# Performance work log

Measured on AMD Instinct MI355X. Metric: run time of the kernel, lower is better.

Reference implementation:

```python
import jax, jax.numpy as jnp
import numpy as np

N = 50000
E = 800000
L = 0.7
EPS = 1e-12  # torch F.normalize eps


def setup_inputs() -> dict:
    key = jax.random.key(0)
    k1, k2, k3, k4, k5 = jax.random.split(key, 5)
    x = jax.random.normal(k1, (N, 256), dtype=jnp.float32)
    W = jax.random.normal(k2, (256, 128), dtype=jnp.float32) * 0.05
    b = jax.random.normal(k3, (128,), dtype=jnp.float32) * 0.05
    src = jax.random.randint(k4, (E,), 0, N, dtype=jnp.int32)
    dst = jax.random.randint(k5, (E,), 0, N, dtype=jnp.int32)
    return {"x": x, "W": W, "b": b, "src": src, "dst": dst}


def _mean_agg(h, src, dst, denom):
    # DGL copy_u + mean over in-edges: mean_{e:(u->v)} h[u]; zero for isolated nodes
    s = jax.ops.segment_sum(h[src], dst, num_segments=N)  # [N, D]
    return s / denom


def reference(x, W, b, src, dst):
    # MLP: Linear -> relu -> row-wise L2 normalize
    h = jax.nn.relu(x @ W + b)
    h = h / jnp.maximum(jnp.linalg.norm(h, axis=1, keepdims=True), EPS)
    # in-degree for mean (clamped to 1 so isolated nodes give 0, matching DGL)
    deg = jax.ops.segment_sum(jnp.ones((E,), jnp.float32), dst, num_segments=N)
    denom = jnp.maximum(deg, 1.0)[:, None]  # [N,1]
    neigh1 = _mean_agg(h, src, dst, denom)
    neigh2 = _mean_agg(neigh1, src, dst, denom)
    mean_h = L * neigh1 + (1.0 - L) * neigh2
    return (h, mean_h)
```

## Files before the change

### kernel.cpp

```cpp
#include <hip/hip_runtime.h>

#define D_IN 256
#define D_OUT 128
#define NBINS 256
#define NB 256

typedef short bf16x8 __attribute__((ext_vector_type(8)));
typedef float f32x4 __attribute__((ext_vector_type(4)));

__device__ __forceinline__ unsigned short f2bf(float f) {
    unsigned int u = __float_as_uint(f);
    unsigned int r = (u + 0x7FFFu + ((u >> 16) & 1u)) >> 16;
    return (unsigned short)r;
}
__device__ __forceinline__ unsigned int pack2(float a, float b) {
    return (unsigned int)f2bf(a) | ((unsigned int)f2bf(b) << 16);
}
__device__ __forceinline__ void gload_lds16(const void* g, void* l) {
    __builtin_amdgcn_global_load_lds(
        (const __attribute__((address_space(1))) void*)g,
        (__attribute__((address_space(3))) void*)l, 16, 0, 0);
}

__global__ __launch_bounds__(256) void k_wt_b1(const float* __restrict__ W,
                                               unsigned short* __restrict__ wt,
                                               const int* __restrict__ dst, int E, int epb,
                                               int* __restrict__ blockbase) {
    __shared__ int hist[NBINS];
    int t = threadIdx.x;
    if (t < 128) {
        int idx = blockIdx.x * 128 + t;
        wt[idx] = f2bf(W[(idx & 255) * D_OUT + (idx >> 8)]);
    }
    hist[t] = 0;
    __syncthreads();
    int s = blockIdx.x * epb;
    int e = min(s + epb, E);
    for (int i = s + t; i < e; i += 256)
        atomicAdd(&hist[dst[i] >> 8], 1);
    __syncthreads();
    blockbase[blockIdx.x * NBINS + t] = hist[t];
}

__global__ __launch_bounds__(256) void k_csrmlp(
    const int* __restrict__ src, const int* __restrict__ dst, int E, int epb,
    const int* __restrict__ blockbase, int* __restrict__ coarse_cnt,
    int* __restrict__ coarse_base, int* __restrict__ ebuf,
    const float* __restrict__ x, const unsigned short* __restrict__ wt,
    const float* __restrict__ bias, float* __restrict__ h,
    unsigned char* __restrict__ hq, int n, int nmblk) {
    __shared__ char smem[32768];
    const int tid = threadIdx.x;
    const int bid = blockIdx.x;

    if (bid < NB) {
        int* cur  = (int*)smem;
        int* base = (int*)(smem + 1024);
        int* sd   = (int*)(smem + 2048);
        int run = 0, myprefix = 0;
        #pragma unroll 8
        for (int b = 0; b < NB; ++b) {
            int v = blockbase[b * NBINS + tid];
            if (b == bid) myprefix = run;
            run += v;
        }
        sd[tid] = run;
        cur[tid] = 0;
        __syncthreads();
        for (int off = 1; off < 256; off <<= 1) {
            int v = (tid >= off) ? sd[tid - off] : 0;
            __syncthreads();
            sd[tid] += v;
            __syncthreads();
        }
        int cb_excl = sd[tid] - run;
        base[tid] = cb_excl + myprefix;
        if (bid == 0) { coarse_cnt[tid] = run; coarse_base[tid] = cb_excl; }
        __syncthreads();
        const int s = bid * epb, e = min(s + epb, E);
        for (int i = s + tid; i < e; i += 256) {
            int d = dst[i];
            int bin = d >> 8;
            int p = atomicAdd(&cur[bin], 1);
            ebuf[base[bin] + p] = (src[i] & 0xffff) | ((d & 255) << 16);
        }
        return;
    }

    const int tile = bid - NB;
    if (tile >= nmblk) return;
    float* sx = (float*)smem;
    unsigned short* swc = (unsigned short*)(smem + 16384);
    const int wid  = tid >> 6;
    const int lane = tid & 63;
    const int row0 = tile * 64;

    f32x4 acc[8];
    #pragma unroll
    for (int fn = 0; fn < 8; ++fn) acc[fn] = (f32x4){0.f, 0.f, 0.f, 0.f};

    for (int k0 = 0; k0 < D_IN; k0 += 64) {
        __syncthreads();
        #pragma unroll
        for (int i = 0; i < 4; ++i) {
            int bi = i * 4 + wid;
            int chunk = bi * 64 + lane;
            int r  = chunk >> 4;
            int cs = chunk & 15;
            int grow = row0 + r;
            const float* g = x + (size_t)grow * D_IN + k0 + ((cs ^ (r & 7)) << 2);
            if (grow < n) gload_lds16(g, (char*)sx + bi * 1024);
        }
        #pragma unroll
        for (int i = 0; i < 4; ++i) {
            int bi = i * 4 + wid;
            int chunk = bi * 64 + lane;
            int nr = chunk >> 3;
            int cs = chunk & 7;
            const unsigned short* g = wt + nr * D_IN + k0 + ((cs ^ (nr & 7)) << 3);
            gload_lds16(g, (char*)swc + bi * 1024);
        }
        __syncthreads();

        #pragma unroll
        for (int kk = 0; kk < 2; ++kk) {
            int r  = wid * 16 + (lane & 15);
            int cs = kk * 8 + (lane >> 4) * 2;
            float4 a0 = *reinterpret_cast<const float4*>(sx + r * 64 + ((cs ^ (r & 7)) << 2));
            float4 a1 = *reinterpret_cast<const float4*>(sx + r * 64 + (((cs + 1) ^ (r & 7)) << 2));
            union { unsigned int u[4]; bf16x8 v; } af;
            af.u[0] = pack2(a0.x, a0.y);
            af.u[1] = pack2(a0.z, a0.w);
            af.u[2] = pack2(a1.x, a1.y);
            af.u[3] = pack2(a1.z, a1.w);
            #pragma unroll
            for (int fn = 0; fn < 8; ++fn) {
                int nr = fn * 16 + (lane & 15);
                int cb = kk * 4 + (lane >> 4);
                bf16x8 bfrag = *reinterpret_cast<const bf16x8*>(
                    swc + nr * 64 + ((cb ^ (nr & 7)) << 3));
                acc[fn] = __builtin_amdgcn_mfma_f32_16x16x32_bf16(af.v, bfrag, acc[fn], 0, 0, 0);
            }
        }
    }

    float bias_r[8];
    #pragma unroll
    for (int fn = 0; fn < 8; ++fn) bias_r[fn] = bias[fn * 16 + (lane & 15)];
    const int colbase = lane & 15;
    const int rgrp = lane >> 4;
    #pragma unroll
    for (int reg = 0; reg < 4; ++reg) {
        int grow = row0 + wid * 16 + rgrp * 4 + reg;
        float v[8];
        float ss = 0.f;
        #pragma unroll
        for (int fn = 0; fn < 8; ++fn) {
            float t = fmaxf(acc[fn][reg] + bias_r[fn], 0.f);
            v[fn] = t;
            ss += t * t;
        }
        ss += __shfl_xor(ss, 1);
        ss += __shfl_xor(ss, 2);
        ss += __shfl_xor(ss, 4);
        ss += __shfl_xor(ss, 8);
        float sc = 1.f / fmaxf(sqrtf(ss), 1e-12f);
        if (grow < n) {
            #pragma unroll
            for (int fn = 0; fn < 8; ++fn) {
                float o = v[fn] * sc;
                h[(size_t)grow * D_OUT + fn * 16 + colbase] = o;
                hq[(size_t)grow * D_OUT + fn * 16 + colbase] =
                    (unsigned char)(int)rintf(o * 255.f);
            }
        }
    }
}

__global__ __launch_bounds__(256) void k_b4(const int* __restrict__ ebuf,
                                            const int* __restrict__ coarse_cnt,
                                            const int* __restrict__ coarse_base,
                                            int* __restrict__ deg, int* __restrict__ offs,
                                            int* __restrict__ csr, int n) {
    __shared__ int hist[NBINS];
    __shared__ int loffs[NBINS];
    int t = threadIdx.x;
    int bin = blockIdx.x;
    int base = coarse_base[bin];
    int size = coarse_cnt[bin];
    hist[t] = 0;
    __syncthreads();
    for (int i = t; i < size; i += 256)
        atomicAdd(&hist[(ebuf[base + i] >> 16) & 255], 1);
    __syncthreads();
    int h = hist[t];
    loffs[t] = h;
    __syncthreads();
    for (int off = 1; off < 256; off <<= 1) {
        int v = (t >= off) ? loffs[t - off] : 0;
        __syncthreads();
        loffs[t] += v;
        __syncthreads();
    }
    int excl = loffs[t] - h;
    int gdst = bin * 256 + t;
    if (gdst < n) {
        deg[gdst]  = h;
        offs[gdst] = base + excl;
    }
    __syncthreads();
    hist[t] = excl;
    __syncthreads();
    for (int i = t; i < size; i += 256) {
        int pr = ebuf[base + i];
        int p = atomicAdd(&hist[(pr >> 16) & 255], 1);
        csr[base + p] = pr & 0xffff;
    }
}

__global__ __launch_bounds__(256) void k_agg1(const unsigned char* __restrict__ hq,
                                              const int* __restrict__ offs,
                                              const int* __restrict__ deg,
                                              const int* __restrict__ csr,
                                              unsigned char* __restrict__ n1q, int n) {
    int node = (blockIdx.x * blockDim.x + threadIdx.x) >> 5;
    int sub  = threadIdx.x & 31;
    if (node >= n) return;
    int d = deg[node];
    int s = offs[node], e = s + d;
    unsigned int a0 = 0u, a1 = 0u;
    int i = s;
    for (; i + 7 < e; i += 8) {
        #pragma unroll
        for (int j = 0; j < 8; ++j) {
            int u = csr[i + j];
            unsigned int q = *reinterpret_cast<const unsigned int*>(
                hq + (size_t)u * D_OUT + sub * 4);
            a0 += q & 0x00FF00FFu;
            a1 += (q >> 8) & 0x00FF00FFu;
        }
    }
    for (; i < e; ++i) {
        int u = csr[i];
        unsigned int q = *reinterpret_cast<const unsigned int*>(
            hq + (size_t)u * D_OUT + sub * 4);
        a0 += q & 0x00FF00FFu;
        a1 += (q >> 8) & 0x00FF00FFu;
    }
    float inv = 1.f / (float)max(d, 1);
    unsigned int b0 = (unsigned int)(int)rintf((float)(a0 & 0xffffu) * inv);
    unsigned int b1 = (unsigned int)(int)rintf((float)(a1 & 0xffffu) * inv);
    unsigned int b2 = (unsigned int)(int)rintf((float)(a0 >> 16) * inv);
    unsigned int b3 = (unsigned int)(int)rintf((float)(a1 >> 16) * inv);
    *reinterpret_cast<unsigned int*>(n1q + (size_t)node * D_OUT + sub * 4) =
        b0 | (b1 << 8) | (b2 << 16) | (b3 << 24);
}

__global__ __launch_bounds__(256) void k_agg2(const unsigned char* __restrict__ n1q,
                                              const int* __restrict__ offs,
                                              const int* __restrict__ deg,
                                              const int* __restrict__ csr,
                                              float* __restrict__ out_m, int n) {
    int node = (blockIdx.x * blockDim.x + threadIdx.x) >> 5;
    int sub  = threadIdx.x & 31;
    if (node >= n) return;
    int d = deg[node];
    int s = offs[node], e = s + d;
    unsigned int a0 = 0u, a1 = 0u;
    int i = s;
    for (; i + 7 < e; i += 8) {
        #pragma unroll
        for (int j = 0; j < 8; ++j) {
            int u = csr[i + j];
            unsigned int q = *reinterpret_cast<const unsigned int*>(
                n1q + (size_t)u * D_OUT + sub * 4);
            a0 += q & 0x00FF00FFu;
            a1 += (q >> 8) & 0x00FF00FFu;
        }
    }
    for (; i < e; ++i) {
        int u = csr[i];
        unsigned int q = *reinterpret_cast<const unsigned int*>(
            n1q + (size_t)u * D_OUT + sub * 4);
        a0 += q & 0x00FF00FFu;
        a1 += (q >> 8) & 0x00FF00FFu;
    }
    float inv = 1.f / (float)max(d, 1);
    unsigned int own = *reinterpret_cast<const unsigned int*>(
        n1q + (size_t)node * D_OUT + sub * 4);
    const float s255 = 1.f / 255.f;
    float4 o;
    o.x = (0.7f * (float)(own & 0xffu)         + 0.3f * (float)(a0 & 0xffffu) * inv) * s255;
    o.y = (0.7f * (float)((own >> 8) & 0xffu)  + 0.3f * (float)(a1 & 0xffffu) * inv) * s255;
    o.z = (0.7f * (float)((own >> 16) & 0xffu) + 0.3f * (float)(a0 >> 16) * inv) * s255;
    o.w = (0.7f * (float)(own >> 24)           + 0.3f * (float)(a1 >> 16) * inv) * s255;
    *reinterpret_cast<float4*>(out_m + (size_t)node * D_OUT + sub * 4) = o;
}

static inline size_t align_up(size_t v, size_t a) { return (v + a - 1) & ~(a - 1); }

extern "C" void kernel_launch(void* const* d_in, const int* in_sizes, int n_in,
                              void* d_out, int out_size, void* d_ws, size_t ws_size,
                              hipStream_t stream) {
    const float* x  = (const float*)d_in[0];
    const float* W  = (const float*)d_in[1];
    const float* b  = (const float*)d_in[2];
    const int* src  = (const int*)d_in[3];
    const int* dst  = (const int*)d_in[4];

    const int n = in_sizes[0] / D_IN;
    const int E = in_sizes[3];

    float* out_h = (float*)d_out;
    float* out_m = out_h + (size_t)n * D_OUT;

    char* ws = (char*)d_ws;
    size_t off = 0;
    int* coarse_cnt  = (int*)(ws + off); off = align_up(off + NBINS * 4, 256);
    int* coarse_base = (int*)(ws + off); off = align_up(off + NBINS * 4, 256);
    int* blockbase   = (int*)(ws + off); off = align_up(off + (size_t)NBINS * NB * 4, 256);
    int* ebuf        = (int*)(ws + off); off = align_up(off + (size_t)E * 4, 256);
    int* csr         = (int*)(ws + off); off = align_up(off + (size_t)E * 4, 256);
    int* deg         = (int*)(ws + off); off = align_up(off + (size_t)n * 4, 256);
    int* offs        = (int*)(ws + off); off = align_up(off + (size_t)n * 4, 256);
    unsigned short* wt = (unsigned short*)(ws + off); off = align_up(off + (size_t)D_OUT * D_IN * 2, 256);
    unsigned char* hq  = (unsigned char*)(ws + off); off = align_up(off + (size_t)n * D_OUT, 256);
    unsigned char* n1q = (unsigned char*)(ws + off); off = align_up(off + (size_t)n * D_OUT, 256);
    (void)ws_size;

    const int epb = (E + NB - 1) / NB;
    const int nbuckets = (n + 255) / 256;
    const int nmblk = (n + 63) / 64;

    k_wt_b1<<<NB, 256, 0, stream>>>(W, wt, dst, E, epb, blockbase);
    k_csrmlp<<<NB + nmblk, 256, 0, stream>>>(src, dst, E, epb, blockbase,
                                             coarse_cnt, coarse_base, ebuf,
                                             x, wt, b, out_h, hq, n, nmblk);
    k_b4<<<nbuckets, 256, 0, stream>>>(ebuf, coarse_cnt, coarse_base, deg, offs, csr, n);

    const int agg_blocks = (n + 7) / 8;
    k_agg1<<<agg_blocks, 256, 0, stream>>>(hq, offs, deg, csr, n1q, n);
    k_agg2<<<agg_blocks, 256, 0, stream>>>(n1q, offs, deg, csr, out_m, n);
}
```

Measured before the change: 95.46 us.

## Load MLP GEMM operands directly from global memory, dropping LDS staging

The MLP tile path no longer stages x and the bf16 weight tile through shared memory with global_load_lds and barriers. Each lane now reads its A fragment straight from x and its B fragments straight from the transposed weights, relying on cache for the weight reuse across waves. This removes the LDS traffic and __syncthreads and shrinks shared memory to what the CSR blocks need, which may raise occupancy. The cost is many more uncoalesced global/L2 reads of the weights per wave.

```diff
diff --git a/kernel.cpp b/kernel.cpp
--- a/kernel.cpp
+++ b/kernel.cpp
@@ -15,11 +15,6 @@
 }
 __device__ __forceinline__ unsigned int pack2(float a, float b) {
     return (unsigned int)f2bf(a) | ((unsigned int)f2bf(b) << 16);
-}
-__device__ __forceinline__ void gload_lds16(const void* g, void* l) {
-    __builtin_amdgcn_global_load_lds(
-        (const __attribute__((address_space(1))) void*)g,
-        (__attribute__((address_space(3))) void*)l, 16, 0, 0);
 }
 
 __global__ __launch_bounds__(256) void k_wt_b1(const float* __restrict__ W,
@@ -49,7 +44,7 @@
     const float* __restrict__ x, const unsigned short* __restrict__ wt,
     const float* __restrict__ bias, float* __restrict__ h,
     unsigned char* __restrict__ hq, int n, int nmblk) {
-    __shared__ char smem[32768];
+    __shared__ char smem[3072];
     const int tid = threadIdx.x;
     const int bid = blockIdx.x;
 
@@ -89,58 +84,38 @@
 
     const int tile = bid - NB;
     if (tile >= nmblk) return;
-    float* sx = (float*)smem;
-    unsigned short* swc = (unsigned short*)(smem + 16384);
     const int wid  = tid >> 6;
     const int lane = tid & 63;
     const int row0 = tile * 64;
+    const int arow = row0 + wid * 16 + (lane & 15);
+    const bool valid = arow < n;
+    const int kbase = (lane >> 4) << 3;
+    const float* ax = x + (size_t)arow * D_IN + kbase;
+    const unsigned short* bw = wt + (size_t)(lane & 15) * D_IN + kbase;
 
     f32x4 acc[8];
     #pragma unroll
     for (int fn = 0; fn < 8; ++fn) acc[fn] = (f32x4){0.f, 0.f, 0.f, 0.f};
 
-    for (int k0 = 0; k0 < D_IN; k0 += 64) {
-        __syncthreads();
+    #pragma unroll
+    for (int kk = 0; kk < 8; ++kk) {
+        const int ko = kk * 32;
+        float4 a0 = make_float4(0.f, 0.f, 0.f, 0.f);
+        float4 a1 = a0;
+        if (valid) {
+            a0 = *reinterpret_cast<const float4*>(ax + ko);
+            a1 = *reinterpret_cast<const float4*>(ax + ko + 4);
+        }
+        union { unsigned int u[4]; bf16x8 v; } af;
+        af.u[0] = pack2(a0.x, a0.y);
+        af.u[1] = pack2(a0.z, a0.w);
+        af.u[2] = pack2(a1.x, a1.y);
+        af.u[3] = pack2(a1.z, a1.w);
         #pragma unroll
-        for (int i = 0; i < 4; ++i) {
-            int bi = i * 4 + wid;
-            int chunk = bi * 64 + lane;
-            int r  = chunk >> 4;
-            int cs = chunk & 15;
-            int grow = row0 + r;
-            const float* g = x + (size_t)grow * D_IN + k0 + ((cs ^ (r & 7)) << 2);
-            if (grow < n) gload_lds16(g, (char*)sx + bi * 1024);
-        }
-        #pragma unroll
-        for (int i = 0; i < 4; ++i) {
-            int bi = i * 4 + wid;
-            int chunk = bi * 64 + lane;
-            int nr = chunk >> 3;
-            int cs = chunk & 7;
-            const unsigned short* g = wt + nr * D_IN + k0 + ((cs ^ (nr & 7)) << 3);
-            gload_lds16(g, (char*)swc + bi * 1024);
-        }
-        __syncthreads();
-
-        #pragma unroll
-        for (int kk = 0; kk < 2; ++kk) {
-            int r  = wid * 16 + (lane & 15);
-            int cs = kk * 8 + (lane >> 4) * 2;
-            float4 a0 = *reinterpret_cast<const float4*>(sx + r * 64 + ((cs ^ (r & 7)) << 2));
-            float4 a1 = *reinterpret_cast<const float4*>(sx + r * 64 + (((cs + 1) ^ (r & 7)) << 2));
-            union { unsigned int u[4]; bf16x8 v; } af;
-            af.u[0] = pack2(a0.x, a0.y);
-            af.u[1] = pack2(a0.z, a0.w);
-            af.u[2] = pack2(a1.x, a1.y);
-            af.u[3] = pack2(a1.z, a1.w);
-            #pragma unroll
-            for (int fn = 0; fn < 8; ++fn) {
-                int nr = fn * 16 + (lane & 15);
-                int cb = kk * 4 + (lane >> 4);
-                bf16x8 bfrag = *reinterpret_cast<const bf16x8*>(
-                    swc + nr * 64 + ((cb ^ (nr & 7)) << 3));
-                acc[fn] = __builtin_amdgcn_mfma_f32_16x16x32_bf16(af.v, bfrag, acc[fn], 0, 0, 0);
-            }
+        for (int fn = 0; fn < 8; ++fn) {
+            bf16x8 bfrag = *reinterpret_cast<const bf16x8*>(
+                bw + (size_t)fn * 16 * D_IN + ko);
+            acc[fn] = __builtin_amdgcn_mfma_f32_16x16x32_bf16(af.v, bfrag, acc[fn], 0, 0, 0);
         }
     }
 
```

Result: slower. 115.2 us (+20.7%).
